# Kernel optimization log

Measured on AMD Instinct MI355X. Metric: run time of the kernel, lower is better.

The kernel has to match this reference:

```python
import jax, jax.numpy as jnp
import numpy as np

ENC_DIM = 256
DEC_DIM = 256
INT_DIM = 256


def setup_inputs() -> dict:
    key = jax.random.key(0)
    k1, k2, k3, k4, k5 = jax.random.split(key, 5)
    B, T = 64, 2048
    encoder_states = jax.random.normal(k1, (B, T, ENC_DIM), dtype=jnp.float32)
    decoder_state = jax.random.normal(k2, (B, DEC_DIM), dtype=jnp.float32)
    s1 = 1.0 / np.sqrt(ENC_DIM)
    s2 = 1.0 / np.sqrt(DEC_DIM)
    s3 = 1.0 / np.sqrt(INT_DIM)
    w1 = jax.random.uniform(k3, (INT_DIM, ENC_DIM), jnp.float32, -s1, s1)
    w2 = jax.random.uniform(k4, (INT_DIM, DEC_DIM), jnp.float32, -s2, s2)
    v = jax.random.uniform(k5, (1, INT_DIM), jnp.float32, -s3, s3)
    return {"encoder_states": encoder_states, "decoder_state": decoder_state,
            "w1": w1, "w2": w2, "v": v}


def reference(encoder_states, decoder_state, w1, w2, v):
    # scores: v @ tanh(W1 e_t + W2 d) for all t at once
    enc_proj = jnp.einsum('bte,ie->bti', encoder_states, w1)      # [B,T,I]
    dec_proj = jnp.einsum('bd,id->bi', decoder_state, w2)          # [B,I]
    scores = jnp.einsum('bti,oi->bt', jnp.tanh(enc_proj + dec_proj[:, None, :]), v)  # [B,T]
    attention_probs = jax.nn.softmax(scores, axis=1)[:, :, None]   # [B,T,1]
    final_context_vec = jnp.sum(attention_probs * encoder_states, axis=1)  # [B,E]
    return final_context_vec, attention_probs
```

## Files before the change

### kernel.cpp

```cpp
#include <hip/hip_runtime.h>
#include <hip/hip_bf16.h>
#include <math.h>

#define Bq 64
#define Tq 2048
#define Eq 256
#define Dq 256
#define Iq 256

using short8  = __attribute__((ext_vector_type(8))) short;
using floatx4 = __attribute__((ext_vector_type(4))) float;

__device__ __forceinline__ float fast_tanh(float x) {
    float e = __expf(2.0f * x);
    return fmaf(-2.0f, __builtin_amdgcn_rcpf(e + 1.0f), 1.0f);
}

__device__ __forceinline__ ushort f2bf(float x) {
    union { __hip_bfloat16 h; ushort u; } c;
    c.h = __float2bfloat16(x);
    return c.u;
}

__device__ __forceinline__ void async_load16(const void* g, void* l) {
    __builtin_amdgcn_global_load_lds(
        (const __attribute__((address_space(1))) void*)g,
        (__attribute__((address_space(3))) void*)l, 16, 0, 0);
}

__global__ __launch_bounds__(256) void prep_kernel(
    const float* __restrict__ w1, ushort* __restrict__ w1sw,
    const float* __restrict__ dec, const float* __restrict__ w2,
    float* __restrict__ dproj)
{
    if (blockIdx.x < 32) {
        const int kc = blockIdx.x;
        const int i  = threadIdx.x;
        const float* src = w1 + i * Eq + kc * 8;
        float4 f0 = *(const float4*)src;
        float4 f1 = *(const float4*)(src + 4);
        ushort u[8] = { f2bf(f0.x), f2bf(f0.y), f2bf(f0.z), f2bf(f0.w),
                        f2bf(f1.x), f2bf(f1.y), f2bf(f1.z), f2bf(f1.w) };
        *(short8*)&w1sw[(kc * 256 + i) * 8] = *(short8*)u;
    } else {
        const int b = blockIdx.x - 32;
        const int i = threadIdx.x;
        __shared__ float dls[Dq];
        dls[i] = dec[b * Dq + i];
        __syncthreads();
        const float* w2r = w2 + i * Dq;
        float acc = 0.f;
        #pragma unroll 8
        for (int d = 0; d < Dq; d += 4) {
            float4 wv = *(const float4*)&w2r[d];
            float4 dv = *(const float4*)&dls[d];
            acc += wv.x * dv.x + wv.y * dv.y + wv.z * dv.z + wv.w * dv.w;
        }
        dproj[b * Iq + i] = acc;
    }
}

__global__ __launch_bounds__(256, 4) void scores_ctx_kernel(
    const float*  __restrict__ enc,
    const ushort* __restrict__ w1sw,
    const float*  __restrict__ v,
    const float*  __restrict__ dproj,
    float* __restrict__ escore,
    float* __restrict__ ctxp,
    float* __restrict__ denomp)
{
    const int b   = blockIdx.y;
    const int bx  = blockIdx.x;
    const int t0  = bx * 64;
    const int tid = threadIdx.x;
    const int w   = tid >> 6;
    const int l   = tid & 63;
    const int l15 = l & 15;
    const int lq  = l >> 4;

    __shared__ alignas(16) float Af[2][64 * 64];
    __shared__ float vls[Iq], dls[Iq];
    __shared__ float swred[4 * 64];

    vls[tid] = v[tid];
    dls[tid] = dproj[b * Iq + tid];

    floatx4 acc[4][4];
    #pragma unroll
    for (int mi = 0; mi < 4; ++mi)
        #pragma unroll
        for (int ni = 0; ni < 4; ++ni)
            acc[mi][ni] = (floatx4)0.f;

    const float* encB = enc + ((size_t)b * Tq + t0) * Eq;

    const int rS = w * 4 + lq;
    const int cS = l15 ^ rS;
    #define STAGE(kt, buf)                                                   \
        _Pragma("unroll")                                                    \
        for (int q = 0; q < 4; ++q) {                                        \
            const int r = q * 16 + rS;                                       \
            async_load16(encB + (size_t)r * Eq + (kt) * 64 + cS * 4,         \
                         &Af[buf][(q * 256 + w * 64) * 4]);                  \
        }

    STAGE(0, 0);
    __syncthreads();

    const ushort* vb = w1sw + ((w * 64 + l15) * 8 + lq * 2048);

    #pragma unroll
    for (int k0i = 0; k0i < 4; ++k0i) {
        const int cur = k0i & 1;
        if (k0i < 3) { STAGE(k0i + 1, cur ^ 1); }

        #pragma unroll
        for (int ks = 0; ks < 2; ++ks) {
            short8 bfv[4];
            #pragma unroll
            for (int ni = 0; ni < 4; ++ni)
                bfv[ni] = *(const short8*)(vb + (k0i * 8 + ks * 4) * 2048 + ni * 128);

            short8 af[4];
            #pragma unroll
            for (int mi = 0; mi < 4; ++mi) {
                const int rr = mi * 16 + l15;
                const int s0 = (ks * 8 + lq * 2) ^ l15;
                const int s1 = s0 ^ 1;
                float4 f0 = *(const float4*)&Af[cur][rr * 64 + s0 * 4];
                float4 f1 = *(const float4*)&Af[cur][rr * 64 + s1 * 4];
                ushort u[8] = { f2bf(f0.x), f2bf(f0.y), f2bf(f0.z), f2bf(f0.w),
                                f2bf(f1.x), f2bf(f1.y), f2bf(f1.z), f2bf(f1.w) };
                af[mi] = *(short8*)u;
            }

            __builtin_amdgcn_s_setprio(1);
            #pragma unroll
            for (int mi = 0; mi < 4; ++mi)
                #pragma unroll
                for (int ni = 0; ni < 4; ++ni)
                    acc[mi][ni] = __builtin_amdgcn_mfma_f32_16x16x32_bf16(
                        af[mi], bfv[ni], acc[mi][ni], 0, 0, 0);
            __builtin_amdgcn_s_setprio(0);
        }
        if (k0i < 3) __syncthreads();
    }

    float part[4][4];
    #pragma unroll
    for (int mi = 0; mi < 4; ++mi)
        #pragma unroll
        for (int r = 0; r < 4; ++r) part[mi][r] = 0.f;

    #pragma unroll
    for (int ni = 0; ni < 4; ++ni) {
        const int i    = w * 64 + ni * 16 + l15;
        const float vi = vls[i];
        const float dp = dls[i];
        #pragma unroll
        for (int mi = 0; mi < 4; ++mi)
            #pragma unroll
            for (int r = 0; r < 4; ++r)
                part[mi][r] += vi * fast_tanh(acc[mi][ni][r] + dp);
    }

    #pragma unroll
    for (int mi = 0; mi < 4; ++mi)
        #pragma unroll
        for (int r = 0; r < 4; ++r) {
            float x = part[mi][r];
            x += __shfl_xor(x, 1); x += __shfl_xor(x, 2);
            x += __shfl_xor(x, 4); x += __shfl_xor(x, 8);
            part[mi][r] = x;
        }
    if (l15 == 0) {
        #pragma unroll
        for (int mi = 0; mi < 4; ++mi)
            #pragma unroll
            for (int r = 0; r < 4; ++r)
                swred[w * 64 + mi * 16 + lq * 4 + r] = part[mi][r];
    }
    __syncthreads();

    float s = swred[l] + swred[64 + l] + swred[128 + l] + swred[192 + l];
    const float es = __expf(s);
    if (w == 0) {
        escore[(size_t)b * Tq + t0 + l] = es;
        float tot = es;
        tot += __shfl_xor(tot, 1);  tot += __shfl_xor(tot, 2);
        tot += __shfl_xor(tot, 4);  tot += __shfl_xor(tot, 8);
        tot += __shfl_xor(tot, 16); tot += __shfl_xor(tot, 32);
        if (l == 0) denomp[bx * Bq + b] = tot;
    }

    const int el = l * 4;
    float4 a = {0.f, 0.f, 0.f, 0.f};
    #pragma unroll 8
    for (int tt = 0; tt < 16; ++tt) {
        const int t = w * 16 + tt;
        const float pt = __shfl(es, t);
        float4 ev = *(const float4*)&encB[t * Eq + el];
        a.x += pt * ev.x; a.y += pt * ev.y; a.z += pt * ev.z; a.w += pt * ev.w;
    }
    float* redf = (float*)&Af[0][0];
    *(float4*)&redf[w * 256 + el] = a;
    __syncthreads();
    if (w == 0) {
        float4 a0 = *(const float4*)&redf[0 * 256 + el];
        float4 a1 = *(const float4*)&redf[1 * 256 + el];
        float4 a2 = *(const float4*)&redf[2 * 256 + el];
        float4 a3 = *(const float4*)&redf[3 * 256 + el];
        float4 o;
        o.x = a0.x + a1.x + a2.x + a3.x;
        o.y = a0.y + a1.y + a2.y + a3.y;
        o.z = a0.z + a1.z + a2.z + a3.z;
        o.w = a0.w + a1.w + a2.w + a3.w;
        *(float4*)&ctxp[((size_t)bx * Bq + b) * Eq + el] = o;
    }
}

__global__ __launch_bounds__(256) void finalize_kernel(
    const float* __restrict__ ctxp, const float* __restrict__ denomp,
    float* __restrict__ probs, float* __restrict__ ctx)
{
    const int b   = blockIdx.x;
    const int tid = threadIdx.x;

    float d = denomp[(tid & 31) * Bq + b];
    d += __shfl_xor(d, 1);  d += __shfl_xor(d, 2);  d += __shfl_xor(d, 4);
    d += __shfl_xor(d, 8);  d += __shfl_xor(d, 16);
    const float inv = 1.0f / d;

    float* prow = probs + (size_t)b * Tq + tid * 8;
    float4 p0 = *(const float4*)(prow + 0);
    float4 p1 = *(const float4*)(prow + 4);
    p0.x *= inv; p0.y *= inv; p0.z *= inv; p0.w *= inv;
    p1.x *= inv; p1.y *= inv; p1.z *= inv; p1.w *= inv;
    *(float4*)(prow + 0) = p0;
    *(float4*)(prow + 4) = p1;

    float s = 0.f;
    #pragma unroll 8
    for (int c = 0; c < 32; ++c)
        s += ctxp[((size_t)c * Bq + b) * Eq + tid];
    ctx[b * Eq + tid] = s * inv;
}

extern "C" void kernel_launch(void* const* d_in, const int* in_sizes, int n_in,
                              void* d_out, int out_size, void* d_ws, size_t ws_size,
                              hipStream_t stream) {
    const float* enc = (const float*)d_in[0];
    const float* dec = (const float*)d_in[1];
    const float* w1  = (const float*)d_in[2];
    const float* w2  = (const float*)d_in[3];
    const float* v   = (const float*)d_in[4];

    float* out   = (float*)d_out;
    float* ctx   = out;
    float* probs = out + Bq * Eq;

    char* ws = (char*)d_ws;
    float*  ctxp   = (float*)ws;
    float*  denomp = (float*)(ws + (32*Bq*Eq)*4);
    float*  dproj  = (float*)(ws + (32*Bq*Eq)*4 + 32*Bq*4);
    ushort* w1sw   = (ushort*)(ws + (32*Bq*Eq)*4 + 32*Bq*4 + Bq*Iq*4);

    prep_kernel<<<dim3(96), dim3(256), 0, stream>>>(w1, w1sw, dec, w2, dproj);
    scores_ctx_kernel<<<dim3(Tq / 64, Bq), dim3(256), 0, stream>>>(
        enc, w1sw, v, dproj, probs, ctxp, denomp);
    finalize_kernel<<<dim3(Bq), dim3(256), 0, stream>>>(ctxp, denomp, probs, ctx);
}
```

Baseline: 225.9 us.

## Load encoder A-fragments directly from global instead of LDS double buffering

Removes the async global-to-LDS double-buffered staging of encoder tiles and has each wave read its A fragments straight from global memory into registers before converting to bf16. The v and dproj values are also held in registers instead of shared memory. This drops most LDS use and the per-k-step barriers, which could raise occupancy. In exchange, each of the four waves re-reads the same encoder rows from global/L2, so there is no shared reuse and no overlap of loads with MFMA work.

```diff
diff --git a/kernel.cpp b/kernel.cpp
--- a/kernel.cpp
+++ b/kernel.cpp
@@ -20,12 +20,6 @@
     union { __hip_bfloat16 h; ushort u; } c;
     c.h = __float2bfloat16(x);
     return c.u;
-}
-
-__device__ __forceinline__ void async_load16(const void* g, void* l) {
-    __builtin_amdgcn_global_load_lds(
-        (const __attribute__((address_space(1))) void*)g,
-        (__attribute__((address_space(3))) void*)l, 16, 0, 0);
 }
 
 __global__ __launch_bounds__(256) void prep_kernel(
@@ -78,12 +72,16 @@
     const int l15 = l & 15;
     const int lq  = l >> 4;
 
-    __shared__ alignas(16) float Af[2][64 * 64];
-    __shared__ float vls[Iq], dls[Iq];
     __shared__ float swred[4 * 64];
-
-    vls[tid] = v[tid];
-    dls[tid] = dproj[b * Iq + tid];
+    __shared__ float redf[4 * 256];
+
+    float vv[4], dd[4];
+    #pragma unroll
+    for (int ni = 0; ni < 4; ++ni) {
+        const int i = w * 64 + ni * 16 + l15;
+        vv[ni] = v[i];
+        dd[ni] = dproj[b * Iq + i];
+    }
 
     floatx4 acc[4][4];
     #pragma unroll
@@ -93,46 +91,27 @@
             acc[mi][ni] = (floatx4)0.f;
 
     const float* encB = enc + ((size_t)b * Tq + t0) * Eq;
-
-    const int rS = w * 4 + lq;
-    const int cS = l15 ^ rS;
-    #define STAGE(kt, buf)                                                   \
-        _Pragma("unroll")                                                    \
-        for (int q = 0; q < 4; ++q) {                                        \
-            const int r = q * 16 + rS;                                       \
-            async_load16(encB + (size_t)r * Eq + (kt) * 64 + cS * 4,         \
-                         &Af[buf][(q * 256 + w * 64) * 4]);                  \
-        }
-
-    STAGE(0, 0);
-    __syncthreads();
-
-    const ushort* vb = w1sw + ((w * 64 + l15) * 8 + lq * 2048);
+    const float*  aRow = encB + (size_t)l15 * Eq + lq * 8;
+    const ushort* vb   = w1sw + (w * 64 + l15) * 8 + lq * 2048;
 
     #pragma unroll
     for (int k0i = 0; k0i < 4; ++k0i) {
-        const int cur = k0i & 1;
-        if (k0i < 3) { STAGE(k0i + 1, cur ^ 1); }
-
         #pragma unroll
         for (int ks = 0; ks < 2; ++ks) {
-            short8 bfv[4];
-            #pragma unroll
-            for (int ni = 0; ni < 4; ++ni)
-                bfv[ni] = *(const short8*)(vb + (k0i * 8 + ks * 4) * 2048 + ni * 128);
-
             short8 af[4];
             #pragma unroll
             for (int mi = 0; mi < 4; ++mi) {
-                const int rr = mi * 16 + l15;
-                const int s0 = (ks * 8 + lq * 2) ^ l15;
-                const int s1 = s0 ^ 1;
-                float4 f0 = *(const float4*)&Af[cur][rr * 64 + s0 * 4];
-                float4 f1 = *(const float4*)&Af[cur][rr * 64 + s1 * 4];
+                const float* p = aRow + (size_t)mi * 16 * Eq + k0i * 64 + ks * 32;
+                float4 f0 = *(const float4*)p;
+                float4 f1 = *(const float4*)(p + 4);
                 ushort u[8] = { f2bf(f0.x), f2bf(f0.y), f2bf(f0.z), f2bf(f0.w),
                                 f2bf(f1.x), f2bf(f1.y), f2bf(f1.z), f2bf(f1.w) };
                 af[mi] = *(short8*)u;
             }
+            short8 bfv[4];
+            #pragma unroll
+            for (int ni = 0; ni < 4; ++ni)
+                bfv[ni] = *(const short8*)(vb + (k0i * 8 + ks * 4) * 2048 + ni * 128);
 
             __builtin_amdgcn_s_setprio(1);
             #pragma unroll
@@ -143,7 +122,6 @@
                         af[mi], bfv[ni], acc[mi][ni], 0, 0, 0);
             __builtin_amdgcn_s_setprio(0);
         }
-        if (k0i < 3) __syncthreads();
     }
 
     float part[4][4];
@@ -154,9 +132,8 @@
 
     #pragma unroll
     for (int ni = 0; ni < 4; ++ni) {
-        const int i    = w * 64 + ni * 16 + l15;
-        const float vi = vls[i];
-        const float dp = dls[i];
+        const float vi = vv[ni];
+        const float dp = dd[ni];
         #pragma unroll
         for (int mi = 0; mi < 4; ++mi)
             #pragma unroll
@@ -202,7 +179,6 @@
         float4 ev = *(const float4*)&encB[t * Eq + el];
         a.x += pt * ev.x; a.y += pt * ev.y; a.z += pt * ev.z; a.w += pt * ev.w;
     }
-    float* redf = (float*)&Af[0][0];
     *(float4*)&redf[w * 256 + el] = a;
     __syncthreads();
     if (w == 0) {
```

Result: slower. 247.9 us (+9.8%).
